# Optimization experiments

Measured on AMD Instinct MI355X. Metric: run time of the kernel, lower is better.

Reference implementation:

```python
import jax, jax.numpy as jnp
import numpy as np

N, E = 20000, 320000
FX, FW, FH, H = 256, 128, 128, 4  # x feat, walk feat, hidden=end_embd, heads


def _gat(x, edge_index, W, a_s, a_d, R):
    # W: [H,Fin,Fout]; a_s,a_d: [H,Fout]; R: [Fin,Fout] residual projection
    n = x.shape[0]
    h = jnp.einsum('nf,hfo->hno', x, W)                      # [H,N,Fout]
    src, dst = edge_index[0], edge_index[1]
    s_src = jnp.einsum('hno,ho->nh', h, a_s)                 # [N,H]
    s_dst = jnp.einsum('hno,ho->nh', h, a_d)                 # [N,H]
    e = jax.nn.leaky_relu(s_src[src] + s_dst[dst], 0.2)      # [E,H] per-edge scores
    m = jax.ops.segment_max(e, src, num_segments=n)          # scatter-softmax (stable)
    ex = jnp.exp(e - m[src])
    den = jax.ops.segment_sum(ex, src, num_segments=n)
    alpha = ex / (den[src] + 1e-16)                          # [E,H]
    msg = jnp.transpose(h, (1, 0, 2))[dst] * alpha[:, :, None]        # [E,H,Fout]
    agg = jax.ops.segment_sum(msg, src, num_segments=n).mean(axis=1)  # [N,Fout]
    return jax.nn.elu(agg + x @ R)


def _forward(x, dat, W1, a1s, a1d, R1, W2, a2s, a2d, R2,
             Wd1, ad1s, ad1d, Rd1, Wd2, ad2s, ad2d, Rd2,
             fc1_w, fc1_b, fc2_w, fc2_b, conv_w, conv_b, edge_index):
    x1 = _gat(x, edge_index, W1, a1s, a1d, R1)
    x2 = _gat(x1, edge_index, W2, a2s, a2d, R2)
    d1 = _gat(dat, edge_index, Wd1, ad1s, ad1d, Rd1)
    d2 = _gat(d1, edge_index, Wd2, ad2s, ad2d, Rd2)
    n = x.shape[0]
    # cat on feature dim, transpose, view(1, l*2, end_size, N)
    xd = jnp.concatenate([x1, x2, d1, d2], axis=1).T.reshape(1, 4, FH, n)
    avg = xd.mean(axis=(2, 3))                               # SE global avg pool [1,4]
    att = jax.nn.sigmoid((avg @ fc1_w + fc1_b) @ fc2_w + fc2_b)  # no act between fc1/fc2 (as in source)
    xatt = jax.nn.relu(att[:, :, None, None] * xd)
    y = jnp.einsum('bchn,c->bhn', xatt, conv_w) + conv_b     # 1x1 conv, 4->1 channels
    return y.reshape(FH, n).T                                # dropout = identity (eval)


def setup_inputs():
    key = jax.random.key(0)
    ks = jax.random.split(key, 26)

    def rn(k, shape, s=0.1):
        return jax.random.normal(k, shape, jnp.float32) * s

    return {
        'x': jax.random.normal(ks[0], (N, FX), jnp.float32),
        'dat': jax.random.normal(ks[1], (N, FW), jnp.float32),
        'W1': rn(ks[2], (H, FX, FH)), 'a1s': rn(ks[3], (H, FH)), 'a1d': rn(ks[4], (H, FH)), 'R1': rn(ks[5], (FX, FH)),
        'W2': rn(ks[6], (H, FH, FH)), 'a2s': rn(ks[7], (H, FH)), 'a2d': rn(ks[8], (H, FH)), 'R2': rn(ks[9], (FH, FH)),
        'Wd1': rn(ks[10], (H, FW, FH)), 'ad1s': rn(ks[11], (H, FH)), 'ad1d': rn(ks[12], (H, FH)), 'Rd1': rn(ks[13], (FW, FH)),
        'Wd2': rn(ks[14], (H, FH, FH)), 'ad2s': rn(ks[15], (H, FH)), 'ad2d': rn(ks[16], (H, FH)), 'Rd2': rn(ks[17], (FH, FH)),
        'fc1_w': rn(ks[18], (4, 20)), 'fc1_b': jnp.zeros((20,), jnp.float32),
        'fc2_w': rn(ks[19], (20, 4)), 'fc2_b': jnp.zeros((4,), jnp.float32),
        'conv_w': rn(ks[20], (4,)), 'conv_b': jnp.zeros((), jnp.float32),
        'edge_index': jax.random.randint(ks[21], (2, E), 0, N, dtype=jnp.int32),
    }


def reference(x, dat, W1, a1s, a1d, R1, W2, a2s, a2d, R2,
              Wd1, ad1s, ad1d, Rd1, Wd2, ad2s, ad2d, Rd2,
              fc1_w, fc1_b, fc2_w, fc2_b, conv_w, conv_b, edge_index):
    return _forward(x, dat, W1, a1s, a1d, R1, W2, a2s, a2d, R2,
                    Wd1, ad1s, ad1d, Rd1, Wd2, ad2s, ad2d, Rd2,
                    fc1_w, fc1_b, fc2_w, fc2_b, conv_w, conv_b, edge_index)
```

## Files before the change

### kernel.cpp

```cpp
#include <hip/hip_runtime.h>
#include <hip/hip_bf16.h>
#include <math.h>

#define NN 20000
#define EE 320000
#define FXX 256
#define FWW 128
#define NH 4

typedef __attribute__((ext_vector_type(8))) short short8v;
typedef __attribute__((ext_vector_type(4))) float f32x4;

static __device__ __forceinline__ float bf2f(unsigned short s) {
    unsigned int u = ((unsigned int)s) << 16;
    return __builtin_bit_cast(float, u);
}

static __device__ __forceinline__ unsigned short f2bf_u16(float f) {
    unsigned int u = __builtin_bit_cast(unsigned int, f);
    unsigned int r = 0x7fffu + ((u >> 16) & 1u);
    return (unsigned short)((u + r) >> 16);
}

__global__ __launch_bounds__(256) void cast2_kernel(const float* __restrict__ a, __hip_bfloat16* __restrict__ ab, int na,
                                                    const float* __restrict__ b, __hip_bfloat16* __restrict__ bb, int nb)
{
    int i = (blockIdx.x * 256 + threadIdx.x) * 4;
    if (i < na) {
        float4 v = *(const float4*)(a + i);
        ab[i + 0] = __float2bfloat16(v.x); ab[i + 1] = __float2bfloat16(v.y);
        ab[i + 2] = __float2bfloat16(v.z); ab[i + 3] = __float2bfloat16(v.w);
    } else {
        int j = i - na;
        if (j < nb) {
            float4 v = *(const float4*)(b + j);
            bb[j + 0] = __float2bfloat16(v.x); bb[j + 1] = __float2bfloat16(v.y);
            bb[j + 2] = __float2bfloat16(v.z); bb[j + 3] = __float2bfloat16(v.w);
        }
    }
}

struct WscItem { const float* W; const float* as_; const float* ad_; int Fin; };
struct WscParams { WscItem t[4]; };

__global__ __launch_bounds__(256) void wsc_kernel(WscParams p, float* __restrict__ wsc)
{
    int L = blockIdx.z;
    WscItem it = p.t[L];
    int wid = threadIdx.x >> 6, lane = threadIdx.x & 63;
    int r = blockIdx.x * 4 + wid;
    if (r >= it.Fin * 4) return;
    int h = r / it.Fin, k = r - h * it.Fin;
    float2 w2 = *(const float2*)(it.W + ((size_t)(h * it.Fin + k)) * 128 + 2 * lane);
    float2 s2 = *(const float2*)(it.as_ + h * 128 + 2 * lane);
    float2 d2 = *(const float2*)(it.ad_ + h * 128 + 2 * lane);
    float vs = w2.x * s2.x + w2.y * s2.y;
    float vd = w2.x * d2.x + w2.y * d2.y;
    #pragma unroll
    for (int o = 32; o; o >>= 1) { vs += __shfl_xor(vs, o); vd += __shfl_xor(vd, o); }
    if (lane == 0) {
        wsc[(size_t)L * 2048 + h * 256 + k] = vs;
        wsc[(size_t)L * 2048 + (4 + h) * 256 + k] = vd;
    }
}

struct WcItem { const float* W; const float* R; __hip_bfloat16* dst; int Fin; int KK; int total; };
struct WcParams { WcItem t[4]; };

__global__ __launch_bounds__(256) void wcomb_kernel(WcParams p)
{
    WcItem it = p.t[blockIdx.z];
    int idx = blockIdx.x * 256 + threadIdx.x;
    if (idx >= it.total) return;
    int c = idx / it.KK;
    int k5 = idx - c * it.KK;
    int f4 = it.Fin * 4;
    float v;
    if (k5 < f4) {
        int h = k5 / it.Fin, k = k5 - h * it.Fin;
        v = 0.25f * it.W[((size_t)(h * it.Fin + k)) * 128 + c];
    } else {
        v = it.R[(size_t)(k5 - f4) * 128 + c];
    }
    it.dst[(size_t)c * it.KK + k5] = __float2bfloat16(v);
}

template<int CF>
__global__ __launch_bounds__(256) void score_kernel(const __hip_bfloat16* __restrict__ Xb,
                                                    const float* __restrict__ wsc,
                                                    float* __restrict__ ssrc,
                                                    float* __restrict__ sdst)
{
    const int Fin = CF * 64;
    int wid = threadIdx.x >> 6, lane = threadIdx.x & 63;
    int n = blockIdx.x * 4 + wid;
    if (n >= NN) return;
    int c0 = lane * CF;
    union { unsigned u[CF / 2]; unsigned short s[CF]; } ld;
    #pragma unroll
    for (int w = 0; w < CF / 2; ++w)
        ld.u[w] = *(const unsigned*)(Xb + (size_t)n * Fin + c0 + w * 2);
    float xv[CF];
    #pragma unroll
    for (int i = 0; i < CF; ++i) xv[i] = bf2f(ld.s[i]);
    float acc[8];
    #pragma unroll
    for (int j = 0; j < 8; ++j) {
        const float* w = wsc + j * 256 + c0;
        float s = 0.f;
        #pragma unroll
        for (int i = 0; i < CF; ++i) s += xv[i] * w[i];
        acc[j] = s;
    }
    #pragma unroll
    for (int o = 32; o; o >>= 1)
        #pragma unroll
        for (int j = 0; j < 8; ++j) acc[j] += __shfl_xor(acc[j], o);
    if (lane == 0) {
        *(float4*)(ssrc + (size_t)n * 4) = make_float4(acc[0], acc[1], acc[2], acc[3]);
        *(float4*)(sdst + (size_t)n * 4) = make_float4(acc[4], acc[5], acc[6], acc[7]);
    }
}

__global__ __launch_bounds__(256) void hist_kernel(const int* __restrict__ src, int* __restrict__ cnt)
{
    int i = blockIdx.x * blockDim.x + threadIdx.x;
    if (i < EE) atomicAdd(&cnt[src[i]], 1);
}

__global__ __launch_bounds__(1024) void scan_kernel(const int* __restrict__ cnt, int* __restrict__ row_ptr)
{
    __shared__ int lds[1024];
    int t = threadIdx.x;
    const int CH = 20;
    int start = t * CH, end = start + CH; if (end > NN) end = NN;
    int sum = 0;
    if (start < NN) for (int i = start; i < end; ++i) sum += cnt[i];
    lds[t] = sum;
    __syncthreads();
    for (int o = 1; o < 1024; o <<= 1) {
        int v = (t >= o) ? lds[t - o] : 0;
        __syncthreads();
        lds[t] += v;
        __syncthreads();
    }
    int run = lds[t] - sum;
    if (start < NN) for (int i = start; i < end; ++i) { row_ptr[i] = run; run += cnt[i]; }
    if (t == 1023) row_ptr[NN] = lds[1023];
}

__global__ __launch_bounds__(256) void scatter_kernel(const int* __restrict__ src,
                                                      const int* __restrict__ dst,
                                                      const int* __restrict__ row_ptr,
                                                      int* __restrict__ off,
                                                      int* __restrict__ csr_dst)
{
    int i = blockIdx.x * blockDim.x + threadIdx.x;
    if (i >= EE) return;
    int s = src[i];
    int p = row_ptr[s] + atomicAdd(&off[s], 1);
    csr_dst[p] = dst[i];
}

template<int CF>
__global__ __launch_bounds__(256) void agg_cat_kernel(const __hip_bfloat16* __restrict__ Xb,
                                                      const float* __restrict__ ssrc,
                                                      const float* __restrict__ sdst,
                                                      const int* __restrict__ row_ptr,
                                                      const int* __restrict__ csr_dst,
                                                      __hip_bfloat16* __restrict__ Cat)
{
    const int Fin = CF * 64, KK = 5 * Fin;
    int wid = threadIdx.x >> 6, lane = threadIdx.x & 63;
    int n = blockIdx.x * 4 + wid;
    if (n >= NN) return;
    int r0 = row_ptr[n], r1 = row_ptr[n + 1];
    int deg = r1 - r0;

    float acc[4][CF] = {};

    if (deg > 0) {
        float4 sn = *(const float4*)(ssrc + (size_t)n * 4);
        auto comp_e = [&](int s, int& dout) -> float4 {
            int d = csr_dst[r0 + s];
            dout = d;
            float4 sd = *(const float4*)(sdst + (size_t)d * 4);
            float4 e; float v;
            v = sn.x + sd.x; e.x = v >= 0.f ? v : 0.2f * v;
            v = sn.y + sd.y; e.y = v >= 0.f ? v : 0.2f * v;
            v = sn.z + sd.z; e.z = v >= 0.f ? v : 0.2f * v;
            v = sn.w + sd.w; e.w = v >= 0.f ? v : 0.2f * v;
            return e;
        };

        float4 e0 = make_float4(-1e30f, -1e30f, -1e30f, -1e30f);
        int d0 = 0;
        if (lane < deg) e0 = comp_e(lane, d0);
        float4 m = e0;
        for (int s = lane + 64; s < deg; s += 64) {
            int dt; float4 ev = comp_e(s, dt);
            m.x = fmaxf(m.x, ev.x); m.y = fmaxf(m.y, ev.y);
            m.z = fmaxf(m.z, ev.z); m.w = fmaxf(m.w, ev.w);
        }
        #pragma unroll
        for (int o = 32; o; o >>= 1) {
            m.x = fmaxf(m.x, __shfl_xor(m.x, o));
            m.y = fmaxf(m.y, __shfl_xor(m.y, o));
            m.z = fmaxf(m.z, __shfl_xor(m.z, o));
            m.w = fmaxf(m.w, __shfl_xor(m.w, o));
        }
        float4 p0 = make_float4(0.f, 0.f, 0.f, 0.f);
        if (lane < deg) {
            p0.x = expf(e0.x - m.x); p0.y = expf(e0.y - m.y);
            p0.z = expf(e0.z - m.z); p0.w = expf(e0.w - m.w);
        }
        float4 den = p0;
        for (int s = lane + 64; s < deg; s += 64) {
            int dt; float4 ev = comp_e(s, dt);
            den.x += expf(ev.x - m.x); den.y += expf(ev.y - m.y);
            den.z += expf(ev.z - m.z); den.w += expf(ev.w - m.w);
        }
        #pragma unroll
        for (int o = 32; o; o >>= 1) {
            den.x += __shfl_xor(den.x, o); den.y += __shfl_xor(den.y, o);
            den.z += __shfl_xor(den.z, o); den.w += __shfl_xor(den.w, o);
        }
        den.x = 1.f / (den.x + 1e-16f); den.y = 1.f / (den.y + 1e-16f);
        den.z = 1.f / (den.z + 1e-16f); den.w = 1.f / (den.w + 1e-16f);

        float4 a0;
        a0.x = p0.x * den.x; a0.y = p0.y * den.y;
        a0.z = p0.z * den.z; a0.w = p0.w * den.w;

        int cnt0 = min(deg, 64);
        int last = cnt0 - 1;
        for (int base = 0; base < cnt0; base += 4) {
            int j1 = min(base + 1, last), j2 = min(base + 2, last), j3 = min(base + 3, last);
            int dv0 = __shfl(d0, base), dv1 = __shfl(d0, j1);
            int dv2 = __shfl(d0, j2),   dv3 = __shfl(d0, j3);
            union U { unsigned u[CF / 2]; unsigned short s[CF]; };
            U l0, l1, l2, l3;
            #pragma unroll
            for (int w = 0; w < CF / 2; ++w)
                l0.u[w] = *(const unsigned*)(Xb + (size_t)dv0 * Fin + lane * CF + w * 2);
            #pragma unroll
            for (int w = 0; w < CF / 2; ++w)
                l1.u[w] = *(const unsigned*)(Xb + (size_t)dv1 * Fin + lane * CF + w * 2);
            #pragma unroll
            for (int w = 0; w < CF / 2; ++w)
                l2.u[w] = *(const unsigned*)(Xb + (size_t)dv2 * Fin + lane * CF + w * 2);
            #pragma unroll
            for (int w = 0; w < CF / 2; ++w)
                l3.u[w] = *(const unsigned*)(Xb + (size_t)dv3 * Fin + lane * CF + w * 2);

            {
                float ax = __shfl(a0.x, base), ay = __shfl(a0.y, base);
                float az = __shfl(a0.z, base), aw = __shfl(a0.w, base);
                #pragma unroll
                for (int i = 0; i < CF; ++i) {
                    float xv = bf2f(l0.s[i]);
                    acc[0][i] += ax * xv; acc[1][i] += ay * xv;
                    acc[2][i] += az * xv; acc[3][i] += aw * xv;
                }
            }
            if (base + 1 < cnt0) {
                float ax = __shfl(a0.x, j1), ay = __shfl(a0.y, j1);
                float az = __shfl(a0.z, j1), aw = __shfl(a0.w, j1);
                #pragma unroll
                for (int i = 0; i < CF; ++i) {
                    float xv = bf2f(l1.s[i]);
                    acc[0][i] += ax * xv; acc[1][i] += ay * xv;
                    acc[2][i] += az * xv; acc[3][i] += aw * xv;
                }
            }
            if (base + 2 < cnt0) {
                float ax = __shfl(a0.x, j2), ay = __shfl(a0.y, j2);
                float az = __shfl(a0.z, j2), aw = __shfl(a0.w, j2);
                #pragma unroll
                for (int i = 0; i < CF; ++i) {
                    float xv = bf2f(l2.s[i]);
                    acc[0][i] += ax * xv; acc[1][i] += ay * xv;
                    acc[2][i] += az * xv; acc[3][i] += aw * xv;
                }
            }
            if (base + 3 < cnt0) {
                float ax = __shfl(a0.x, j3), ay = __shfl(a0.y, j3);
                float az = __shfl(a0.z, j3), aw = __shfl(a0.w, j3);
                #pragma unroll
                for (int i = 0; i < CF; ++i) {
                    float xv = bf2f(l3.s[i]);
                    acc[0][i] += ax * xv; acc[1][i] += ay * xv;
                    acc[2][i] += az * xv; acc[3][i] += aw * xv;
                }
            }
        }

        for (int r = r0 + 64; r < r1; r += 64) {
            int cnt = min(64, r1 - r);
            int d = 0;
            float4 a4 = make_float4(0.f, 0.f, 0.f, 0.f);
            if (r + lane < r1) {
                int dt;
                float4 ev = comp_e(r - r0 + lane, dt);
                d = dt;
                a4.x = expf(ev.x - m.x) * den.x; a4.y = expf(ev.y - m.y) * den.y;
                a4.z = expf(ev.z - m.z) * den.z; a4.w = expf(ev.w - m.w) * den.w;
            }
            for (int j = 0; j < cnt; ++j) {
                int ddv = __shfl(d, j);
                float ax = __shfl(a4.x, j), ay = __shfl(a4.y, j);
                float az = __shfl(a4.z, j), aw = __shfl(a4.w, j);
                union { unsigned u[CF / 2]; unsigned short s[CF]; } ld;
                #pragma unroll
                for (int w = 0; w < CF / 2; ++w)
                    ld.u[w] = *(const unsigned*)(Xb + (size_t)ddv * Fin + lane * CF + w * 2);
                #pragma unroll
                for (int i = 0; i < CF; ++i) {
                    float xv = bf2f(ld.s[i]);
                    acc[0][i] += ax * xv; acc[1][i] += ay * xv;
                    acc[2][i] += az * xv; acc[3][i] += aw * xv;
                }
            }
        }
    }

    __hip_bfloat16* crow = Cat + (size_t)n * KK;
    #pragma unroll
    for (int h = 0; h < 4; ++h) {
        union { unsigned u[CF / 2]; unsigned short s[CF]; } pk;
        #pragma unroll
        for (int i = 0; i < CF; ++i) pk.s[i] = f2bf_u16(acc[h][i]);
        #pragma unroll
        for (int w = 0; w < CF / 2; ++w)
            *(unsigned*)(crow + h * Fin + lane * CF + w * 2) = pk.u[w];
    }
    #pragma unroll
    for (int w = 0; w < CF / 2; ++w)
        *(unsigned*)(crow + 4 * Fin + lane * CF + w * 2) =
            *(const unsigned*)(Xb + (size_t)n * Fin + lane * CF + w * 2);
}

template<int KK>
__global__ __launch_bounds__(256) void gemm_elu(const __hip_bfloat16* __restrict__ Cat,
                                                const __hip_bfloat16* __restrict__ Wct,
                                                float* __restrict__ xout,
                                                __hip_bfloat16* __restrict__ xbout,
                                                float* __restrict__ sums, int ch)
{
    const int BK = 64;
    const int NIT = KK / BK;
    __shared__ short As[2][32 * 72];
    __shared__ short Bs[2][128 * 72];
    __shared__ float ls[4];

    int tid = threadIdx.x, lane = tid & 63, wid = tid >> 6;
    int wr = wid >> 1, wc = wid & 1;
    int ar = lane & 15, kg = lane >> 4;
    int row0 = blockIdx.x * 32;

    int a_row = tid >> 3, a_seg = tid & 7;
    int b_col = tid >> 1, b_seg0 = (tid & 1) * 4;

    const __hip_bfloat16* Ag = Cat + (size_t)(row0 + a_row) * KK + a_seg * 8;
    const __hip_bfloat16* Bg = Wct + (size_t)b_col * KK + b_seg0 * 8;

    short8v fa, fb0, fb1, fb2, fb3;

    f32x4 acc[4] = {};

    fa  = *(const short8v*)(Ag);
    fb0 = *(const short8v*)(Bg);
    fb1 = *(const short8v*)(Bg + 8);
    fb2 = *(const short8v*)(Bg + 16);
    fb3 = *(const short8v*)(Bg + 24);
    *(short8v*)(&As[0][a_row * 72 + a_seg * 8]) = fa;
    *(short8v*)(&Bs[0][b_col * 72 + (b_seg0 + 0) * 8]) = fb0;
    *(short8v*)(&Bs[0][b_col * 72 + (b_seg0 + 1) * 8]) = fb1;
    *(short8v*)(&Bs[0][b_col * 72 + (b_seg0 + 2) * 8]) = fb2;
    *(short8v*)(&Bs[0][b_col * 72 + (b_seg0 + 3) * 8]) = fb3;

    int cur = 0;
    for (int it = 0; it < NIT; ++it) {
        if (it + 1 < NIT) {
            int kb = (it + 1) * BK;
            fa  = *(const short8v*)(Ag + kb);
            fb0 = *(const short8v*)(Bg + kb);
            fb1 = *(const short8v*)(Bg + kb + 8);
            fb2 = *(const short8v*)(Bg + kb + 16);
            fb3 = *(const short8v*)(Bg + kb + 24);
        }
        __syncthreads();
        #pragma unroll
        for (int ks = 0; ks < 2; ++ks) {
            short8v a = *(const short8v*)(&As[cur][(wr * 16 + ar) * 72 + ks * 32 + kg * 8]);
            #pragma unroll
            for (int nb = 0; nb < 4; ++nb) {
                short8v b = *(const short8v*)(&Bs[cur][(wc * 64 + nb * 16 + ar) * 72 + ks * 32 + kg * 8]);
                acc[nb] = __builtin_amdgcn_mfma_f32_16x16x32_bf16(a, b, acc[nb], 0, 0, 0);
            }
        }
        if (it + 1 < NIT) {
            int nb2 = cur ^ 1;
            *(short8v*)(&As[nb2][a_row * 72 + a_seg * 8]) = fa;
            *(short8v*)(&Bs[nb2][b_col * 72 + (b_seg0 + 0) * 8]) = fb0;
            *(short8v*)(&Bs[nb2][b_col * 72 + (b_seg0 + 1) * 8]) = fb1;
            *(short8v*)(&Bs[nb2][b_col * 72 + (b_seg0 + 2) * 8]) = fb2;
            *(short8v*)(&Bs[nb2][b_col * 72 + (b_seg0 + 3) * 8]) = fb3;
        }
        cur ^= 1;
    }

    float lsum = 0.f;
    int rsub = (lane >> 4) * 4;
    #pragma unroll
    for (int nb = 0; nb < 4; ++nb) {
        int col = wc * 64 + nb * 16 + ar;
        #pragma unroll
        for (int r = 0; r < 4; ++r) {
            int row = row0 + wr * 16 + rsub + r;
            float v = acc[nb][r];
            v = v > 0.f ? v : expm1f(v);
            lsum += v;
            xout[(size_t)row * 128 + col] = v;
            xbout[(size_t)row * 128 + col] = __float2bfloat16(v);
        }
    }
    #pragma unroll
    for (int o = 32; o; o >>= 1) lsum += __shfl_xor(lsum, o);
    if (lane == 0) ls[wid] = lsum;
    __syncthreads();
    if (tid == 0) atomicAdd(&sums[ch], ls[0] + ls[1] + ls[2] + ls[3]);
}

__global__ void att_kernel(const float* __restrict__ sums,
                           const float* __restrict__ fc1w, const float* __restrict__ fc1b,
                           const float* __restrict__ fc2w, const float* __restrict__ fc2b,
                           float* __restrict__ att)
{
    if (threadIdx.x != 0 || blockIdx.x != 0) return;
    float avg[4];
    for (int c = 0; c < 4; ++c) avg[c] = sums[c] * (1.f / (NN * 128.f));
    float z[20];
    for (int j = 0; j < 20; ++j) {
        float v = fc1b[j];
        for (int c = 0; c < 4; ++c) v += avg[c] * fc1w[c * 20 + j];
        z[j] = v;
    }
    for (int c = 0; c < 4; ++c) {
        float v = fc2b[c];
        for (int j = 0; j < 20; ++j) v += z[j] * fc2w[j * 4 + c];
        att[c] = 1.f / (1.f + expf(-v));
    }
}

__global__ __launch_bounds__(256) void final_kernel(const float* __restrict__ x1,
                                                    const float* __restrict__ x2,
                                                    const float* __restrict__ d1,
                                                    const float* __restrict__ d2,
                                                    const float* __restrict__ att,
                                                    const float* __restrict__ convw,
                                                    const float* __restrict__ convb,
                                                    float* __restrict__ out)
{
    int i = blockIdx.x * blockDim.x + threadIdx.x;
    if (i >= NN * 128) return;
    float a0 = att[0], a1 = att[1], a2 = att[2], a3 = att[3];
    float w0 = convw[0], w1 = convw[1], w2 = convw[2], w3 = convw[3];
    float v = convb[0];
    v += w0 * fmaxf(a0 * x1[i], 0.f);
    v += w1 * fmaxf(a1 * x2[i], 0.f);
    v += w2 * fmaxf(a2 * d1[i], 0.f);
    v += w3 * fmaxf(a3 * d2[i], 0.f);
    out[i] = v;
}

extern "C" void kernel_launch(void* const* d_in, const int* in_sizes, int n_in,
                              void* d_out, int out_size, void* d_ws, size_t ws_size,
                              hipStream_t stream)
{
    (void)in_sizes; (void)n_in; (void)out_size; (void)ws_size;
    const float* x    = (const float*)d_in[0];
    const float* dat  = (const float*)d_in[1];
    const float* W1   = (const float*)d_in[2];
    const float* a1s  = (const float*)d_in[3];
    const float* a1d  = (const float*)d_in[4];
    const float* R1   = (const float*)d_in[5];
    const float* W2   = (const float*)d_in[6];
    const float* a2s  = (const float*)d_in[7];
    const float* a2d  = (const float*)d_in[8];
    const float* R2   = (const float*)d_in[9];
    const float* Wd1  = (const float*)d_in[10];
    const float* ad1s = (const float*)d_in[11];
    const float* ad1d = (const float*)d_in[12];
    const float* Rd1  = (const float*)d_in[13];
    const float* Wd2  = (const float*)d_in[14];
    const float* ad2s = (const float*)d_in[15];
    const float* ad2d = (const float*)d_in[16];
    const float* Rd2  = (const float*)d_in[17];
    const float* fc1w = (const float*)d_in[18];
    const float* fc1b = (const float*)d_in[19];
    const float* fc2w = (const float*)d_in[20];
    const float* fc2b = (const float*)d_in[21];
    const float* convw= (const float*)d_in[22];
    const float* convb= (const float*)d_in[23];
    const int*   eidx = (const int*)d_in[24];
    const int* esrc = eidx;
    const int* edst = eidx + EE;
    float* out = (float*)d_out;

    char* base = (char*)d_ws;
    size_t woff = 0;
    auto alloc = [&](size_t bytes) -> void* {
        void* p = base + woff;
        woff = (woff + bytes + 255) & ~(size_t)255;
        return p;
    };
    __hip_bfloat16* Cat  = (__hip_bfloat16*)alloc((size_t)NN * 1280 * 2);
    float* X1    = (float*)alloc((size_t)NN * 128 * 4);
    float* X2    = (float*)alloc((size_t)NN * 128 * 4);
    float* D1    = (float*)alloc((size_t)NN * 128 * 4);
    float* D2    = (float*)alloc((size_t)NN * 128 * 4);
    __hip_bfloat16* XbX   = (__hip_bfloat16*)alloc((size_t)NN * FXX * 2);
    __hip_bfloat16* XbDat = (__hip_bfloat16*)alloc((size_t)NN * FWW * 2);
    __hip_bfloat16* Xb1   = (__hip_bfloat16*)alloc((size_t)NN * 128 * 2);
    __hip_bfloat16* XbD1  = (__hip_bfloat16*)alloc((size_t)NN * 128 * 2);
    __hip_bfloat16* XbTmp = (__hip_bfloat16*)alloc((size_t)NN * 128 * 2);
    float* Wsc   = (float*)alloc((size_t)4 * 2048 * 4);
    __hip_bfloat16* Wct0 = (__hip_bfloat16*)alloc((size_t)128 * 1280 * 2);
    __hip_bfloat16* Wct1 = (__hip_bfloat16*)alloc((size_t)128 * 640 * 2);
    __hip_bfloat16* Wct2 = (__hip_bfloat16*)alloc((size_t)128 * 640 * 2);
    __hip_bfloat16* Wct3 = (__hip_bfloat16*)alloc((size_t)128 * 640 * 2);
    float* Ssrc  = (float*)alloc((size_t)NN * 4 * 4);
    float* Sdst  = (float*)alloc((size_t)NN * 4 * 4);
    int* RowPtr  = (int*)alloc((size_t)(NN + 1) * 4);
    int* Cnt     = (int*)alloc((size_t)NN * 4);
    int* Off     = (int*)alloc((size_t)NN * 4);
    int* CsrDst  = (int*)alloc((size_t)EE * 4);
    float* Sums  = (float*)alloc(16);
    float* Att   = (float*)alloc(16);

    {
        int na = NN * FXX, nb = NN * FWW;
        cast2_kernel<<<(na + nb + 1023) / 1024, 256, 0, stream>>>(x, XbX, na, dat, XbDat, nb);
        WscParams WP;
        WP.t[0] = { W1,  a1s,  a1d,  FXX };
        WP.t[1] = { W2,  a2s,  a2d,  FWW };
        WP.t[2] = { Wd1, ad1s, ad1d, FWW };
        WP.t[3] = { Wd2, ad2s, ad2d, FWW };
        wsc_kernel<<<dim3(256, 1, 4), 256, 0, stream>>>(WP, Wsc);
        WcParams CP;
        CP.t[0] = { W1,  R1,  Wct0, FXX, 1280, 128 * 1280 };
        CP.t[1] = { W2,  R2,  Wct1, FWW, 640,  128 * 640 };
        CP.t[2] = { Wd1, Rd1, Wct2, FWW, 640,  128 * 640 };
        CP.t[3] = { Wd2, Rd2, Wct3, FWW, 640,  128 * 640 };
        wcomb_kernel<<<dim3(640, 1, 4), 256, 0, stream>>>(CP);
    }
    hipMemsetAsync(Cnt, 0, (size_t)NN * 4, stream);
    hipMemsetAsync(Off, 0, (size_t)NN * 4, stream);
    hipMemsetAsync(Sums, 0, 16, stream);
    hist_kernel<<<(EE + 255) / 256, 256, 0, stream>>>(esrc, Cnt);
    scan_kernel<<<1, 1024, 0, stream>>>(Cnt, RowPtr);
    scatter_kernel<<<(EE + 255) / 256, 256, 0, stream>>>(esrc, edst, RowPtr, Off, CsrDst);

    auto layer = [&](const __hip_bfloat16* Xb, int CF, int Lidx, int ch,
                     const __hip_bfloat16* WctL, float* xout, __hip_bfloat16* xbout) {
        const float* wscL = Wsc + (size_t)Lidx * 2048;
        if (CF == 4) {
            score_kernel<4><<<(NN + 3) / 4, 256, 0, stream>>>(Xb, wscL, Ssrc, Sdst);
            agg_cat_kernel<4><<<(NN + 3) / 4, 256, 0, stream>>>(Xb, Ssrc, Sdst, RowPtr, CsrDst, Cat);
            gemm_elu<1280><<<NN / 32, 256, 0, stream>>>(Cat, WctL, xout, xbout, Sums, ch);
        } else {
            score_kernel<2><<<(NN + 3) / 4, 256, 0, stream>>>(Xb, wscL, Ssrc, Sdst);
            agg_cat_kernel<2><<<(NN + 3) / 4, 256, 0, stream>>>(Xb, Ssrc, Sdst, RowPtr, CsrDst, Cat);
            gemm_elu<640><<<NN / 32, 256, 0, stream>>>(Cat, WctL, xout, xbout, Sums, ch);
        }
    };

    layer(XbX,   4, 0, 0, Wct0, X1, Xb1);
    layer(Xb1,   2, 1, 1, Wct1, X2, XbTmp);
    layer(XbDat, 2, 2, 2, Wct2, D1, XbD1);
    layer(XbD1,  2, 3, 3, Wct3, D2, XbTmp);

    att_kernel<<<1, 64, 0, stream>>>(Sums, fc1w, fc1b, fc2w, fc2b, Att);
    final_kernel<<<(NN * 128 + 255) / 256, 256, 0, stream>>>(X1, X2, D1, D2, Att, convw, convb, out);
}
```

Measured before the change: 364.8 us.

## Fuse bf16 cast into score kernel and next-layer scores into GEMM epilogue

```diff
diff --git a/kernel.cpp b/kernel.cpp
--- a/kernel.cpp
+++ b/kernel.cpp
@@ -20,24 +20,6 @@
     unsigned int u = __builtin_bit_cast(unsigned int, f);
     unsigned int r = 0x7fffu + ((u >> 16) & 1u);
     return (unsigned short)((u + r) >> 16);
-}
-
-__global__ __launch_bounds__(256) void cast2_kernel(const float* __restrict__ a, __hip_bfloat16* __restrict__ ab, int na,
-                                                    const float* __restrict__ b, __hip_bfloat16* __restrict__ bb, int nb)
-{
-    int i = (blockIdx.x * 256 + threadIdx.x) * 4;
-    if (i < na) {
-        float4 v = *(const float4*)(a + i);
-        ab[i + 0] = __float2bfloat16(v.x); ab[i + 1] = __float2bfloat16(v.y);
-        ab[i + 2] = __float2bfloat16(v.z); ab[i + 3] = __float2bfloat16(v.w);
-    } else {
-        int j = i - na;
-        if (j < nb) {
-            float4 v = *(const float4*)(b + j);
-            bb[j + 0] = __float2bfloat16(v.x); bb[j + 1] = __float2bfloat16(v.y);
-            bb[j + 2] = __float2bfloat16(v.z); bb[j + 3] = __float2bfloat16(v.w);
-        }
-    }
 }
 
 struct WscItem { const float* W; const float* as_; const float* ad_; int Fin; };
@@ -86,23 +68,26 @@
 }
 
 template<int CF>
-__global__ __launch_bounds__(256) void score_kernel(const __hip_bfloat16* __restrict__ Xb,
-                                                    const float* __restrict__ wsc,
-                                                    float* __restrict__ ssrc,
-                                                    float* __restrict__ sdst)
+__global__ __launch_bounds__(256) void cast_score(const float* __restrict__ Xf,
+                                                  __hip_bfloat16* __restrict__ Xb,
+                                                  const float* __restrict__ wsc,
+                                                  float* __restrict__ ssrc,
+                                                  float* __restrict__ sdst)
 {
     const int Fin = CF * 64;
     int wid = threadIdx.x >> 6, lane = threadIdx.x & 63;
     int n = blockIdx.x * 4 + wid;
     if (n >= NN) return;
     int c0 = lane * CF;
-    union { unsigned u[CF / 2]; unsigned short s[CF]; } ld;
+    float xv[CF];
+    #pragma unroll
+    for (int i = 0; i < CF; ++i) xv[i] = Xf[(size_t)n * Fin + c0 + i];
+    union { unsigned u[CF / 2]; unsigned short s[CF]; } pk;
+    #pragma unroll
+    for (int i = 0; i < CF; ++i) pk.s[i] = f2bf_u16(xv[i]);
     #pragma unroll
     for (int w = 0; w < CF / 2; ++w)
-        ld.u[w] = *(const unsigned*)(Xb + (size_t)n * Fin + c0 + w * 2);
-    float xv[CF];
-    #pragma unroll
-    for (int i = 0; i < CF; ++i) xv[i] = bf2f(ld.s[i]);
+        *(unsigned*)(Xb + (size_t)n * Fin + c0 + w * 2) = pk.u[w];
     float acc[8];
     #pragma unroll
     for (int j = 0; j < 8; ++j) {
@@ -170,7 +155,7 @@
                                                       const int* __restrict__ csr_dst,
                                                       __hip_bfloat16* __restrict__ Cat)
 {
-    const int Fin = CF * 64, KK = 5 * Fin;
+    const int Fin = CF * 64, F4 = 4 * Fin;
     int wid = threadIdx.x >> 6, lane = threadIdx.x & 63;
     int n = blockIdx.x * 4 + wid;
     if (n >= NN) return;
@@ -324,7 +309,7 @@
         }
     }
 
-    __hip_bfloat16* crow = Cat + (size_t)n * KK;
+    __hip_bfloat16* crow = Cat + (size_t)n * F4;
     #pragma unroll
     for (int h = 0; h < 4; ++h) {
         union { unsigned u[CF / 2]; unsigned short s[CF]; } pk;
@@ -334,24 +319,26 @@
         for (int w = 0; w < CF / 2; ++w)
             *(unsigned*)(crow + h * Fin + lane * CF + w * 2) = pk.u[w];
     }
-    #pragma unroll
-    for (int w = 0; w < CF / 2; ++w)
-        *(unsigned*)(crow + 4 * Fin + lane * CF + w * 2) =
-            *(const unsigned*)(Xb + (size_t)n * Fin + lane * CF + w * 2);
-}
-
-template<int KK>
+}
+
+template<int F4, int FIN, bool DOSC>
 __global__ __launch_bounds__(256) void gemm_elu(const __hip_bfloat16* __restrict__ Cat,
+                                                const __hip_bfloat16* __restrict__ Xb,
                                                 const __hip_bfloat16* __restrict__ Wct,
                                                 float* __restrict__ xout,
                                                 __hip_bfloat16* __restrict__ xbout,
-                                                float* __restrict__ sums, int ch)
-{
+                                                float* __restrict__ sums, int ch,
+                                                const float* __restrict__ wscN,
+                                                float* __restrict__ ssrcN,
+                                                float* __restrict__ sdstN)
+{
+    const int KK = F4 + FIN;
     const int BK = 64;
     const int NIT = KK / BK;
     __shared__ short As[2][32 * 72];
     __shared__ short Bs[2][128 * 72];
     __shared__ float ls[4];
+    __shared__ float sred[4][4][4][8];
 
     int tid = threadIdx.x, lane = tid & 63, wid = tid >> 6;
     int wr = wid >> 1, wc = wid & 1;
@@ -361,14 +348,14 @@
     int a_row = tid >> 3, a_seg = tid & 7;
     int b_col = tid >> 1, b_seg0 = (tid & 1) * 4;
 
-    const __hip_bfloat16* Ag = Cat + (size_t)(row0 + a_row) * KK + a_seg * 8;
+    const __hip_bfloat16* AgC = Cat + (size_t)(row0 + a_row) * F4 + a_seg * 8;
+    const __hip_bfloat16* AgX = Xb + (size_t)(row0 + a_row) * FIN + a_seg * 8;
     const __hip_bfloat16* Bg = Wct + (size_t)b_col * KK + b_seg0 * 8;
 
     short8v fa, fb0, fb1, fb2, fb3;
-
     f32x4 acc[4] = {};
 
-    fa  = *(const short8v*)(Ag);
+    fa  = *(const short8v*)(AgC);
     fb0 = *(const short8v*)(Bg);
     fb1 = *(const short8v*)(Bg + 8);
     fb2 = *(const short8v*)(Bg + 16);
@@ -383,7 +370,7 @@
     for (int it = 0; it < NIT; ++it) {
         if (it + 1 < NIT) {
             int kb = (it + 1) * BK;
-            fa  = *(const short8v*)(Ag + kb);
+            fa  = (kb < F4) ? *(const short8v*)(AgC + kb) : *(const short8v*)(AgX + (kb - F4));
             fb0 = *(const short8v*)(Bg + kb);
             fb1 = *(const short8v*)(Bg + kb + 8);
             fb2 = *(const short8v*)(Bg + kb + 16);
@@ -411,6 +398,7 @@
     }
 
     float lsum = 0.f;
+    float vpost[4][4];
     int rsub = (lane >> 4) * 4;
     #pragma unroll
     for (int nb = 0; nb < 4; ++nb) {
@@ -420,6 +408,7 @@
             int row = row0 + wr * 16 + rsub + r;
             float v = acc[nb][r];
             v = v > 0.f ? v : expm1f(v);
+            vpost[nb][r] = v;
             lsum += v;
             xout[(size_t)row * 128 + col] = v;
             xbout[(size_t)row * 128 + col] = __float2bfloat16(v);
@@ -428,8 +417,42 @@
     #pragma unroll
     for (int o = 32; o; o >>= 1) lsum += __shfl_xor(lsum, o);
     if (lane == 0) ls[wid] = lsum;
+
+    if (DOSC) {
+        float sc[4][8] = {};
+        #pragma unroll
+        for (int j = 0; j < 8; ++j) {
+            #pragma unroll
+            for (int nb = 0; nb < 4; ++nb) {
+                float wv = wscN[j * 256 + wc * 64 + nb * 16 + ar];
+                #pragma unroll
+                for (int r = 0; r < 4; ++r) sc[r][j] += vpost[nb][r] * wv;
+            }
+        }
+        #pragma unroll
+        for (int o = 8; o; o >>= 1)
+            #pragma unroll
+            for (int r = 0; r < 4; ++r)
+                #pragma unroll
+                for (int j = 0; j < 8; ++j) sc[r][j] += __shfl_xor(sc[r][j], o);
+        if (ar == 0) {
+            int grp = lane >> 4;
+            #pragma unroll
+            for (int r = 0; r < 4; ++r)
+                #pragma unroll
+                for (int j = 0; j < 8; ++j) sred[wid][grp][r][j] = sc[r][j];
+        }
+    }
     __syncthreads();
     if (tid == 0) atomicAdd(&sums[ch], ls[0] + ls[1] + ls[2] + ls[3]);
+    if (DOSC) {
+        int row_local = tid >> 3, j = tid & 7;
+        int w_r = row_local >> 4, grp = (row_local >> 2) & 3, r = row_local & 3;
+        float total = sred[w_r * 2 + 0][grp][r][j] + sred[w_r * 2 + 1][grp][r][j];
+        int row = row0 + row_local;
+        if (j < 4) ssrcN[(size_t)row * 4 + j] = total;
+        else       sdstN[(size_t)row * 4 + (j - 4)] = total;
+    }
 }
 
 __global__ void att_kernel(const float* __restrict__ sums,
@@ -515,7 +538,7 @@
         woff = (woff + bytes + 255) & ~(size_t)255;
         return p;
     };
-    __hip_bfloat16* Cat  = (__hip_bfloat16*)alloc((size_t)NN * 1280 * 2);
+    __hip_bfloat16* Cat  = (__hip_bfloat16*)alloc((size_t)NN * 1024 * 2);
     float* X1    = (float*)alloc((size_t)NN * 128 * 4);
     float* X2    = (float*)alloc((size_t)NN * 128 * 4);
     float* D1    = (float*)alloc((size_t)NN * 128 * 4);
@@ -530,8 +553,14 @@
     __hip_bfloat16* Wct1 = (__hip_bfloat16*)alloc((size_t)128 * 640 * 2);
     __hip_bfloat16* Wct2 = (__hip_bfloat16*)alloc((size_t)128 * 640 * 2);
     __hip_bfloat16* Wct3 = (__hip_bfloat16*)alloc((size_t)128 * 640 * 2);
-    float* Ssrc  = (float*)alloc((size_t)NN * 4 * 4);
-    float* Sdst  = (float*)alloc((size_t)NN * 4 * 4);
+    float* SsrcX = (float*)alloc((size_t)NN * 4 * 4);
+    float* SdstX = (float*)alloc((size_t)NN * 4 * 4);
+    float* Ssrc1 = (float*)alloc((size_t)NN * 4 * 4);
+    float* Sdst1 = (float*)alloc((size_t)NN * 4 * 4);
+    float* SsrcD = (float*)alloc((size_t)NN * 4 * 4);
+    float* SdstD = (float*)alloc((size_t)NN * 4 * 4);
+    float* Ssrc3 = (float*)alloc((size_t)NN * 4 * 4);
+    float* Sdst3 = (float*)alloc((size_t)NN * 4 * 4);
     int* RowPtr  = (int*)alloc((size_t)(NN + 1) * 4);
     int* Cnt     = (int*)alloc((size_t)NN * 4);
     int* Off     = (int*)alloc((size_t)NN * 4);
@@ -540,8 +569,6 @@
     float* Att   = (float*)alloc(16);
 
     {
-        int na = NN * FXX, nb = NN * FWW;
-        cast2_kernel<<<(na + nb + 1023) / 1024, 256, 0, stream>>>(x, XbX, na, dat, XbDat, nb);
         WscParams WP;
         WP.t[0] = { W1,  a1s,  a1d,  FXX };
         WP.t[1] = { W2,  a2s,  a2d,  FWW };
@@ -554,6 +581,8 @@
         CP.t[2] = { Wd1, Rd1, Wct2, FWW, 640,  128 * 640 };
         CP.t[3] = { Wd2, Rd2, Wct3, FWW, 640,  128 * 640 };
         wcomb_kernel<<<dim3(640, 1, 4), 256, 0, stream>>>(CP);
+        cast_score<4><<<(NN + 3) / 4, 256, 0, stream>>>(x, XbX, Wsc, SsrcX, SdstX);
+        cast_score<2><<<(NN + 3) / 4, 256, 0, stream>>>(dat, XbDat, Wsc + 2 * 2048, SsrcD, SdstD);
     }
     hipMemsetAsync(Cnt, 0, (size_t)NN * 4, stream);
     hipMemsetAsync(Off, 0, (size_t)NN * 4, stream);
@@ -562,24 +591,18 @@
     scan_kernel<<<1, 1024, 0, stream>>>(Cnt, RowPtr);
     scatter_kernel<<<(EE + 255) / 256, 256, 0, stream>>>(esrc, edst, RowPtr, Off, CsrDst);
 
-    auto layer = [&](const __hip_bfloat16* Xb, int CF, int Lidx, int ch,
-                     const __hip_bfloat16* WctL, float* xout, __hip_bfloat16* xbout) {
-        const float* wscL = Wsc + (size_t)Lidx * 2048;
-        if (CF == 4) {
-            score_kernel<4><<<(NN + 3) / 4, 256, 0, stream>>>(Xb, wscL, Ssrc, Sdst);
-            agg_cat_kernel<4><<<(NN + 3) / 4, 256, 0, stream>>>(Xb, Ssrc, Sdst, RowPtr, CsrDst, Cat);
-            gemm_elu<1280><<<NN / 32, 256, 0, stream>>>(Cat, WctL, xout, xbout, Sums, ch);
-        } else {
-            score_kernel<2><<<(NN + 3) / 4, 256, 0, stream>>>(Xb, wscL, Ssrc, Sdst);
-            agg_cat_kernel<2><<<(NN + 3) / 4, 256, 0, stream>>>(Xb, Ssrc, Sdst, RowPtr, CsrDst, Cat);
-            gemm_elu<640><<<NN / 32, 256, 0, stream>>>(Cat, WctL, xout, xbout, Sums, ch);
-        }
-    };
-
-    layer(XbX,   4, 0, 0, Wct0, X1, Xb1);
-    layer(Xb1,   2, 1, 1, Wct1, X2, XbTmp);
-    layer(XbDat, 2, 2, 2, Wct2, D1, XbD1);
-    layer(XbD1,  2, 3, 3, Wct3, D2, XbTmp);
+    agg_cat_kernel<4><<<(NN + 3) / 4, 256, 0, stream>>>(XbX, SsrcX, SdstX, RowPtr, CsrDst, Cat);
+    gemm_elu<1024, 256, true><<<NN / 32, 256, 0, stream>>>(Cat, XbX, Wct0, X1, Xb1, Sums, 0,
+                                                           Wsc + 1 * 2048, Ssrc1, Sdst1);
+    agg_cat_kernel<2><<<(NN + 3) / 4, 256, 0, stream>>>(Xb1, Ssrc1, Sdst1, RowPtr, CsrDst, Cat);
+    gemm_elu<512, 128, false><<<NN / 32, 256, 0, stream>>>(Cat, Xb1, Wct1, X2, XbTmp, Sums, 1,
+                                                           nullptr, nullptr, nullptr);
+    agg_cat_kernel<2><<<(NN + 3) / 4, 256, 0, stream>>>(XbDat, SsrcD, SdstD, RowPtr, CsrDst, Cat);
+    gemm_elu<512, 128, true><<<NN / 32, 256, 0, stream>>>(Cat, XbDat, Wct2, D1, XbD1, Sums, 2,
+                                                          Wsc + 3 * 2048, Ssrc3, Sdst3);
+    agg_cat_kernel<2><<<(NN + 3) / 4, 256, 0, stream>>>(XbD1, Ssrc3, Sdst3, RowPtr, CsrDst, Cat);
+    gemm_elu<512, 128, false><<<NN / 32, 256, 0, stream>>>(Cat, XbD1, Wct3, D2, XbTmp, Sums, 3,
+                                                           nullptr, nullptr, nullptr);
 
     att_kernel<<<1, 64, 0, stream>>>(Sums, fc1w, fc1b, fc2w, fc2b, Att);
     final_kernel<<<(NN * 128 + 255) / 256, 256, 0, stream>>>(X1, X2, D1, D2, Att, convw, convb, out);
```

Result: faster. 339.5 us (-6.9%).
